# Kernel tuning notes

Hardware: AMD Instinct MI355X
Metric: run time of the kernel (lower is better)

The kernel has to match this reference:

```python
import jax, jax.numpy as jnp
import numpy as np

QUERY_SIZE = 128


def setup_inputs() -> dict:
    key = jax.random.key(0)
    ks = jax.random.split(key, 4)
    S, B, T, E, Q = 512, 32, 1024, 512, QUERY_SIZE
    query = jax.random.normal(ks[0], (S, B, Q), dtype=jnp.float32)
    embedded_text = jax.random.normal(ks[1], (T, B, E), dtype=jnp.float32)
    text_mask = jnp.ones((T, B), dtype=jnp.float32)
    position = jnp.zeros((S, B), dtype=jnp.float32)
    # nn.Linear(query_size, 2): W [2, Q], b [2]; kaiming-uniform-ish init scale
    lim = 1.0 / np.sqrt(Q)
    W = jax.random.uniform(ks[2], (2, Q), dtype=jnp.float32, minval=-lim, maxval=lim)
    b = jax.random.uniform(ks[3], (2,), dtype=jnp.float32, minval=-lim, maxval=lim)
    return {"query": query, "embedded_text": embedded_text, "text_mask": text_mask,
            "position": position, "W": W, "b": b}


def reference(query, embedded_text, text_mask, position, W, b):
    # query: [S,B,Q], embedded_text: [T,B,E], text_mask: [T,B], position: [S,B]
    masked_embedding = embedded_text * text_mask[:, :, None]          # [T,B,E]
    query_result = jnp.exp(query @ W.T + b)                           # [S,B,2]
    mean_raw = query_result[..., 0]                                   # [S,B]
    std = query_result[..., 1]                                        # [S,B]
    mean = position + jnp.cumsum(mean_raw, axis=0) / 20.0             # [S,B]
    T = embedded_text.shape[0]
    indices = jnp.arange(T, dtype=query.dtype)                        # [T]
    # Gaussian window weights over text positions: [S,T,B]
    weights = jnp.exp(-std[:, None, :] * (mean[:, None, :] - indices[None, :, None]) ** 2)
    # Reduce over text_len without materializing [S,T,B,E]
    new_context = jnp.einsum('stb,tbe->sbe', weights, masked_embedding)  # [S,B,E]
    return new_context, mean
```

## Files before the change

kernel.cpp:

```cpp
#include <hip/hip_runtime.h>
#include <hip/hip_bf16.h>


#define S_DIM 512
#define B_DIM 32
#define T_DIM 1024
#define E_DIM 512
#define Q_DIM 128
#define WIN_CUT 20.0f


__global__ __launch_bounds__(256) void dot_kernel(
    const float* __restrict__ query,
    const float* __restrict__ W,
    const float* __restrict__ bias,
    float* __restrict__ ws_A,
    float* __restrict__ ws_std)
{
    const int wave = threadIdx.x >> 6;
    const int lane = threadIdx.x & 63;
    const int pair = blockIdx.x * 4 + wave;
    const float2* qp = (const float2*)(query + (size_t)pair * Q_DIM);
    float2 v = qp[lane];
    float d0 = v.x * W[2 * lane]         + v.y * W[2 * lane + 1];
    float d1 = v.x * W[Q_DIM + 2 * lane] + v.y * W[Q_DIM + 2 * lane + 1];
    #pragma unroll
    for (int off = 32; off; off >>= 1) {
        d0 += __shfl_down(d0, off);
        d1 += __shfl_down(d1, off);
    }
    if (lane == 0) {
        int s = pair / B_DIM, b = pair % B_DIM;
        ws_A[(size_t)b * S_DIM + s] = expf(d0 + bias[0]);
        ws_std[pair]                = expf(d1 + bias[1]);
    }
}

__global__ __launch_bounds__(S_DIM) void scan_kernel(
    float* __restrict__ ws_A,
    const float* __restrict__ position,
    float* __restrict__ out_mean)
{
    __shared__ float scan[S_DIM];
    const int b = blockIdx.x;
    const int s = threadIdx.x;
    scan[s] = ws_A[(size_t)b * S_DIM + s];
    __syncthreads();
    for (int off = 1; off < S_DIM; off <<= 1) {
        float v = (s >= off) ? scan[s - off] : 0.f;
        __syncthreads();
        scan[s] += v;
        __syncthreads();
    }
    const size_t idx = (size_t)s * B_DIM + b;
    float mean = position[idx] + scan[s] * 0.05f;
    ws_A[(size_t)b * S_DIM + s] = mean;
    out_mean[idx] = mean;
}

__global__ __launch_bounds__(128) void ctx_kernel(
    const float* __restrict__ emb,
    const float* __restrict__ mask,
    const float* __restrict__ ws_A,
    const float* __restrict__ ws_std,
    float* __restrict__ out)
{
    const int s = blockIdx.x;
    const int b = blockIdx.y;
    const size_t sb = (size_t)s * B_DIM + b;
    const float mean = ws_A[(size_t)b * S_DIM + s];
    const float st   = ws_std[sb];

    const float r = __fsqrt_rn(WIN_CUT / st);
    int tlo = (int)floorf(mean - r); if (tlo < 0) tlo = 0;
    int thi = (int)ceilf(mean + r);  if (thi > T_DIM - 1) thi = T_DIM - 1;

    const int tid = threadIdx.x;
    float a0 = 0.f, a1 = 0.f, a2 = 0.f, a3 = 0.f;
    for (int t = tlo; t <= thi; ++t) {
        float d = mean - (float)t;
        float w = __expf(-st * d * d) * mask[(size_t)t * B_DIM + b];
        const float4* row = (const float4*)(emb + ((size_t)t * B_DIM + b) * E_DIM);
        float4 v = row[tid];
        a0 += w * v.x; a1 += w * v.y; a2 += w * v.z; a3 += w * v.w;
    }
    float4 o; o.x = a0; o.y = a1; o.z = a2; o.w = a3;
    ((float4*)(out + sb * E_DIM))[tid] = o;
}

__global__ __launch_bounds__(1024) void fused_fallback(
    const float* __restrict__ query, const float* __restrict__ emb,
    const float* __restrict__ mask,  const float* __restrict__ position,
    const float* __restrict__ W,     const float* __restrict__ bias,
    float* __restrict__ out_ctx, float* __restrict__ out_mean)
{
    __shared__ float s_mean[S_DIM];
    __shared__ float s_std[S_DIM];
    __shared__ float s_w0[Q_DIM], s_w1[Q_DIM];
    const int b = blockIdx.x;
    const int tid = threadIdx.x;
    if (tid < Q_DIM) { s_w0[tid] = W[tid]; s_w1[tid] = W[Q_DIM + tid]; }
    __syncthreads();

    if (tid < S_DIM) {
        const float4* q4 = (const float4*)(query + ((size_t)tid * B_DIM + b) * Q_DIM);
        float d0 = 0.f, d1 = 0.f;
        #pragma unroll 4
        for (int i = 0; i < Q_DIM / 4; ++i) {
            float4 qv = q4[i];
            d0 += qv.x * s_w0[4*i]   + qv.y * s_w0[4*i+1]
                + qv.z * s_w0[4*i+2] + qv.w * s_w0[4*i+3];
            d1 += qv.x * s_w1[4*i]   + qv.y * s_w1[4*i+1]
                + qv.z * s_w1[4*i+2] + qv.w * s_w1[4*i+3];
        }
        s_mean[tid] = expf(d0 + bias[0]);
        s_std[tid]  = expf(d1 + bias[1]);
    }
    __syncthreads();
    for (int off = 1; off < S_DIM; off <<= 1) {
        float v = 0.f;
        if (tid < S_DIM && tid >= off) v = s_mean[tid - off];
        __syncthreads();
        if (tid < S_DIM) s_mean[tid] += v;
        __syncthreads();
    }
    if (tid < S_DIM) {
        const size_t idx = (size_t)tid * B_DIM + b;
        float m = position[idx] + s_mean[tid] * 0.05f;
        s_mean[tid] = m;
        out_mean[idx] = m;
    }
    __syncthreads();

    const int e4 = tid & 127;
    const int sg = tid >> 7;
    for (int s = sg; s < S_DIM; s += 8) {
        const float m  = s_mean[s];
        const float st = s_std[s];
        const float r = __fsqrt_rn(WIN_CUT / st);
        int tlo = (int)floorf(m - r); if (tlo < 0) tlo = 0;
        int thi = (int)ceilf(m + r);  if (thi > T_DIM - 1) thi = T_DIM - 1;
        float a0 = 0.f, a1 = 0.f, a2 = 0.f, a3 = 0.f;
        for (int t = tlo; t <= thi; ++t) {
            float d = m - (float)t;
            float w = __expf(-st * d * d) * mask[(size_t)t * B_DIM + b];
            const float4* row = (const float4*)(emb + ((size_t)t * B_DIM + b) * E_DIM);
            float4 v = row[e4];
            a0 += w * v.x; a1 += w * v.y; a2 += w * v.z; a3 += w * v.w;
        }
        float4 o; o.x = a0; o.y = a1; o.z = a2; o.w = a3;
        ((float4*)(out_ctx + ((size_t)s * B_DIM + b) * E_DIM))[e4] = o;
    }
}

extern "C" void kernel_launch(void* const* d_in, const int* in_sizes, int n_in,
                              void* d_out, int out_size, void* d_ws, size_t ws_size,
                              hipStream_t stream) {
    const float* query = (const float*)d_in[0];
    const float* emb   = (const float*)d_in[1];
    const float* mask  = (const float*)d_in[2];
    const float* pos   = (const float*)d_in[3];
    const float* W     = (const float*)d_in[4];
    const float* bias  = (const float*)d_in[5];

    float* out_ctx  = (float*)d_out;
    float* out_mean = out_ctx + (size_t)S_DIM * B_DIM * E_DIM;

    const size_t need = (size_t)2 * S_DIM * B_DIM * sizeof(float);
    if (ws_size >= need) {
        float* ws_A   = (float*)d_ws;
        float* ws_std = ws_A + (size_t)S_DIM * B_DIM;
        dot_kernel<<<(S_DIM * B_DIM) / 4, 256, 0, stream>>>(query, W, bias, ws_A, ws_std);
        scan_kernel<<<B_DIM, S_DIM, 0, stream>>>(ws_A, pos, out_mean);
        ctx_kernel<<<dim3(S_DIM, B_DIM), 128, 0, stream>>>(emb, mask, ws_A, ws_std, out_ctx);
    } else {
        fused_fallback<<<B_DIM, 1024, 0, stream>>>(query, emb, mask, pos, W, bias,
                                                   out_ctx, out_mean);
    }
}
```

Measured before the change: 139.8 us.

## Tile context kernel over 16 queries sharing embedding rows via LDS weights

Each ctx block now handles 16 consecutive query positions for one batch element. It computes the union of their Gaussian windows, stages per-segment weights in LDS, and reuses each loaded embedding row across all 16 accumulators. The goal is to cut redundant global reads of embedding rows whose windows overlap. The scan becomes a single-wave shuffle scan, and the fallback path is dropped. The cost is a wider union window, so some weights are near zero, plus 16 float4 accumulators per thread raising register pressure. Dropping the workspace-size check assumes enough scratch space for three arrays.

```diff
diff --git a/kernel.cpp b/kernel.cpp
--- a/kernel.cpp
+++ b/kernel.cpp
@@ -8,13 +8,14 @@
 #define E_DIM 512
 #define Q_DIM 128
 #define WIN_CUT 20.0f
-
+#define CH 16
+#define TSEG 64
 
 __global__ __launch_bounds__(256) void dot_kernel(
     const float* __restrict__ query,
     const float* __restrict__ W,
     const float* __restrict__ bias,
-    float* __restrict__ ws_A,
+    float* __restrict__ ws_mraw,
     float* __restrict__ ws_std)
 {
     const int wave = threadIdx.x >> 6;
@@ -31,126 +32,115 @@
     }
     if (lane == 0) {
         int s = pair / B_DIM, b = pair % B_DIM;
-        ws_A[(size_t)b * S_DIM + s] = expf(d0 + bias[0]);
-        ws_std[pair]                = expf(d1 + bias[1]);
+        ws_mraw[(size_t)b * S_DIM + s] = expf(d0 + bias[0]);
+        ws_std[(size_t)b * S_DIM + s]  = expf(d1 + bias[1]);
     }
 }
 
-__global__ __launch_bounds__(S_DIM) void scan_kernel(
-    float* __restrict__ ws_A,
+__global__ __launch_bounds__(64) void scan_kernel(
+    const float* __restrict__ ws_mraw,
     const float* __restrict__ position,
+    float* __restrict__ ws_mean,
     float* __restrict__ out_mean)
 {
-    __shared__ float scan[S_DIM];
     const int b = blockIdx.x;
-    const int s = threadIdx.x;
-    scan[s] = ws_A[(size_t)b * S_DIM + s];
-    __syncthreads();
-    for (int off = 1; off < S_DIM; off <<= 1) {
-        float v = (s >= off) ? scan[s - off] : 0.f;
-        __syncthreads();
-        scan[s] += v;
-        __syncthreads();
+    const int lane = threadIdx.x;
+    const float4* src = (const float4*)(ws_mraw + (size_t)b * S_DIM + lane * 8);
+    float4 x0 = src[0], x1 = src[1];
+    float v[8] = {x0.x, x0.y, x0.z, x0.w, x1.x, x1.y, x1.z, x1.w};
+    float pre[8], run = 0.f;
+    #pragma unroll
+    for (int j = 0; j < 8; ++j) { run += v[j]; pre[j] = run; }
+    float tot = run, sc = tot;
+    #pragma unroll
+    for (int off = 1; off < 64; off <<= 1) {
+        float u = __shfl_up(sc, off);
+        if (lane >= off) sc += u;
     }
-    const size_t idx = (size_t)s * B_DIM + b;
-    float mean = position[idx] + scan[s] * 0.05f;
-    ws_A[(size_t)b * S_DIM + s] = mean;
-    out_mean[idx] = mean;
+    float excl = sc - tot;
+    #pragma unroll
+    for (int j = 0; j < 8; ++j) {
+        int s = lane * 8 + j;
+        float m = position[(size_t)s * B_DIM + b] + (excl + pre[j]) * 0.05f;
+        ws_mean[(size_t)b * S_DIM + s] = m;
+        out_mean[(size_t)s * B_DIM + b] = m;
+    }
 }
 
 __global__ __launch_bounds__(128) void ctx_kernel(
     const float* __restrict__ emb,
     const float* __restrict__ mask,
-    const float* __restrict__ ws_A,
+    const float* __restrict__ ws_mean,
     const float* __restrict__ ws_std,
     float* __restrict__ out)
 {
-    const int s = blockIdx.x;
-    const int b = blockIdx.y;
-    const size_t sb = (size_t)s * B_DIM + b;
-    const float mean = ws_A[(size_t)b * S_DIM + s];
-    const float st   = ws_std[sb];
+    __shared__ float lds_w[TSEG * CH];
+    __shared__ float lds_mean[CH], lds_std[CH];
+    __shared__ int s_tlo, s_thi;
+    const int c = blockIdx.x, b = blockIdx.y;
+    const int s0 = c * CH;
+    const int tid = threadIdx.x;
 
-    const float r = __fsqrt_rn(WIN_CUT / st);
-    int tlo = (int)floorf(mean - r); if (tlo < 0) tlo = 0;
-    int thi = (int)ceilf(mean + r);  if (thi > T_DIM - 1) thi = T_DIM - 1;
-
-    const int tid = threadIdx.x;
-    float a0 = 0.f, a1 = 0.f, a2 = 0.f, a3 = 0.f;
-    for (int t = tlo; t <= thi; ++t) {
-        float d = mean - (float)t;
-        float w = __expf(-st * d * d) * mask[(size_t)t * B_DIM + b];
-        const float4* row = (const float4*)(emb + ((size_t)t * B_DIM + b) * E_DIM);
-        float4 v = row[tid];
-        a0 += w * v.x; a1 += w * v.y; a2 += w * v.z; a3 += w * v.w;
-    }
-    float4 o; o.x = a0; o.y = a1; o.z = a2; o.w = a3;
-    ((float4*)(out + sb * E_DIM))[tid] = o;
-}
-
-__global__ __launch_bounds__(1024) void fused_fallback(
-    const float* __restrict__ query, const float* __restrict__ emb,
-    const float* __restrict__ mask,  const float* __restrict__ position,
-    const float* __restrict__ W,     const float* __restrict__ bias,
-    float* __restrict__ out_ctx, float* __restrict__ out_mean)
-{
-    __shared__ float s_mean[S_DIM];
-    __shared__ float s_std[S_DIM];
-    __shared__ float s_w0[Q_DIM], s_w1[Q_DIM];
-    const int b = blockIdx.x;
-    const int tid = threadIdx.x;
-    if (tid < Q_DIM) { s_w0[tid] = W[tid]; s_w1[tid] = W[Q_DIM + tid]; }
-    __syncthreads();
-
-    if (tid < S_DIM) {
-        const float4* q4 = (const float4*)(query + ((size_t)tid * B_DIM + b) * Q_DIM);
-        float d0 = 0.f, d1 = 0.f;
-        #pragma unroll 4
-        for (int i = 0; i < Q_DIM / 4; ++i) {
-            float4 qv = q4[i];
-            d0 += qv.x * s_w0[4*i]   + qv.y * s_w0[4*i+1]
-                + qv.z * s_w0[4*i+2] + qv.w * s_w0[4*i+3];
-            d1 += qv.x * s_w1[4*i]   + qv.y * s_w1[4*i+1]
-                + qv.z * s_w1[4*i+2] + qv.w * s_w1[4*i+3];
-        }
-        s_mean[tid] = expf(d0 + bias[0]);
-        s_std[tid]  = expf(d1 + bias[1]);
+    if (tid < CH) {
+        lds_mean[tid] = ws_mean[(size_t)b * S_DIM + s0 + tid];
+        lds_std[tid]  = ws_std[(size_t)b * S_DIM + s0 + tid];
     }
     __syncthreads();
-    for (int off = 1; off < S_DIM; off <<= 1) {
-        float v = 0.f;
-        if (tid < S_DIM && tid >= off) v = s_mean[tid - off];
+    if (tid == 0) {
+        float lo = 1e30f, hi = -1e30f;
+        #pragma unroll
+        for (int i = 0; i < CH; ++i) {
+            float r = __fsqrt_rn(WIN_CUT / lds_std[i]);
+            lo = fminf(lo, lds_mean[i] - r);
+            hi = fmaxf(hi, lds_mean[i] + r);
+        }
+        int tlo = (int)floorf(lo);
+        if (tlo < 0) tlo = 0; if (tlo > T_DIM - 1) tlo = T_DIM - 1;
+        int thi = (int)ceilf(hi);
+        if (thi > T_DIM - 1) thi = T_DIM - 1; if (thi < tlo) thi = tlo;
+        s_tlo = tlo; s_thi = thi;
+    }
+    __syncthreads();
+    const int tlo = s_tlo, thi = s_thi;
+
+    float4 acc[CH];
+    #pragma unroll
+    for (int i = 0; i < CH; ++i) acc[i] = float4{0.f, 0.f, 0.f, 0.f};
+
+    for (int tseg = tlo; tseg <= thi; tseg += TSEG) {
+        {
+            const int toff = tid >> 1;
+            const int ibase = (tid & 1) * 8;
+            const int t = tseg + toff;
+            float mv = 0.f;
+            if (t <= thi) mv = mask[(size_t)t * B_DIM + b];
+            #pragma unroll
+            for (int j = 0; j < 8; ++j) {
+                int i = ibase + j;
+                float d = lds_mean[i] - (float)t;
+                float w = (t <= thi) ? __expf(-lds_std[i] * d * d) * mv : 0.f;
+                lds_w[toff * CH + i] = w;
+            }
+        }
         __syncthreads();
-        if (tid < S_DIM) s_mean[tid] += v;
+        const int tend = (thi < tseg + TSEG - 1) ? thi : (tseg + TSEG - 1);
+        for (int t = tseg; t <= tend; ++t) {
+            const int toff = t - tseg;
+            const float4 v =
+                ((const float4*)(emb + ((size_t)t * B_DIM + b) * E_DIM))[tid];
+            const float* wrow = lds_w + toff * CH;
+            #pragma unroll
+            for (int i = 0; i < CH; ++i) {
+                float w = wrow[i];
+                acc[i].x += w * v.x; acc[i].y += w * v.y;
+                acc[i].z += w * v.z; acc[i].w += w * v.w;
+            }
+        }
         __syncthreads();
     }
-    if (tid < S_DIM) {
-        const size_t idx = (size_t)tid * B_DIM + b;
-        float m = position[idx] + s_mean[tid] * 0.05f;
-        s_mean[tid] = m;
-        out_mean[idx] = m;
-    }
-    __syncthreads();
-
-    const int e4 = tid & 127;
-    const int sg = tid >> 7;
-    for (int s = sg; s < S_DIM; s += 8) {
-        const float m  = s_mean[s];
-        const float st = s_std[s];
-        const float r = __fsqrt_rn(WIN_CUT / st);
-        int tlo = (int)floorf(m - r); if (tlo < 0) tlo = 0;
-        int thi = (int)ceilf(m + r);  if (thi > T_DIM - 1) thi = T_DIM - 1;
-        float a0 = 0.f, a1 = 0.f, a2 = 0.f, a3 = 0.f;
-        for (int t = tlo; t <= thi; ++t) {
-            float d = m - (float)t;
-            float w = __expf(-st * d * d) * mask[(size_t)t * B_DIM + b];
-            const float4* row = (const float4*)(emb + ((size_t)t * B_DIM + b) * E_DIM);
-            float4 v = row[e4];
-            a0 += w * v.x; a1 += w * v.y; a2 += w * v.z; a3 += w * v.w;
-        }
-        float4 o; o.x = a0; o.y = a1; o.z = a2; o.w = a3;
-        ((float4*)(out_ctx + ((size_t)s * B_DIM + b) * E_DIM))[e4] = o;
-    }
+    #pragma unroll
+    for (int i = 0; i < CH; ++i)
+        ((float4*)(out + ((size_t)(s0 + i) * B_DIM + b) * E_DIM))[tid] = acc[i];
 }
 
 extern "C" void kernel_launch(void* const* d_in, const int* in_sizes, int n_in,
@@ -166,15 +156,11 @@
     float* out_ctx  = (float*)d_out;
     float* out_mean = out_ctx + (size_t)S_DIM * B_DIM * E_DIM;
 
-    const size_t need = (size_t)2 * S_DIM * B_DIM * sizeof(float);
-    if (ws_size >= need) {
-        float* ws_A   = (float*)d_ws;
-        float* ws_std = ws_A + (size_t)S_DIM * B_DIM;
-        dot_kernel<<<(S_DIM * B_DIM) / 4, 256, 0, stream>>>(query, W, bias, ws_A, ws_std);
-        scan_kernel<<<B_DIM, S_DIM, 0, stream>>>(ws_A, pos, out_mean);
-        ctx_kernel<<<dim3(S_DIM, B_DIM), 128, 0, stream>>>(emb, mask, ws_A, ws_std, out_ctx);
-    } else {
-        fused_fallback<<<B_DIM, 1024, 0, stream>>>(query, emb, mask, pos, W, bias,
-                                                   out_ctx, out_mean);
-    }
+    float* ws_mraw = (float*)d_ws;
+    float* ws_std  = ws_mraw + (size_t)S_DIM * B_DIM;
+    float* ws_mean = ws_std  + (size_t)S_DIM * B_DIM;
+
+    dot_kernel<<<(S_DIM * B_DIM) / 4, 256, 0, stream>>>(query, W, bias, ws_mraw, ws_std);
+    scan_kernel<<<B_DIM, 64, 0, stream>>>(ws_mraw, pos, ws_mean, out_mean);
+    ctx_kernel<<<dim3(S_DIM / CH, B_DIM), 128, 0, stream>>>(emb, mask, ws_mean, ws_std, out_ctx);
 }
```

Result: faster. 131.4 us, median of 2 (-6.1%).
